# Kernel tuning notes

Measured on AMD Instinct MI355X. Metric: run time of the kernel, lower is better.

## Reference

```python
import jax, jax.numpy as jnp
import numpy as np

N_NODES = 50000
N_EDGES = 800000
IN_FEATS = 64
HIDDEN = 64
NUM_CLASSES = 32


def _graph_conv(x, src, dst, W, b, n_nodes):
    # DGL GraphConv, norm='both', allow_zero_in_degree=True:
    # out = D_in^{-1/2} * (A^T @ (D_out^{-1/2} * x)) @ W + b, degrees clamped to >=1
    e = src.shape[0]
    ones = jnp.ones((e,), dtype=x.dtype)
    out_deg = jax.ops.segment_sum(ones, src, num_segments=n_nodes)
    in_deg = jax.ops.segment_sum(ones, dst, num_segments=n_nodes)
    norm_src = jax.lax.rsqrt(jnp.maximum(out_deg, 1.0))[:, None]
    norm_dst = jax.lax.rsqrt(jnp.maximum(in_deg, 1.0))[:, None]
    h = x * norm_src                                   # [N, d]
    agg = jax.ops.segment_sum(h[src], dst, num_segments=n_nodes)  # gather+scatter over edges
    return (agg * norm_dst) @ W + b


def setup_inputs() -> dict:
    key = jax.random.key(0)
    k1, k2, k3, k4, k5 = jax.random.split(key, 5)
    features = jax.random.normal(k1, (N_NODES, IN_FEATS), dtype=jnp.float32)
    src = jax.random.randint(k2, (N_EDGES,), 0, N_NODES, dtype=jnp.int32)
    dst = jax.random.randint(k3, (N_EDGES,), 0, N_NODES, dtype=jnp.int32)
    W1 = jax.random.normal(k4, (IN_FEATS, HIDDEN), dtype=jnp.float32) * (1.0 / np.sqrt(IN_FEATS))
    b1 = jnp.zeros((HIDDEN,), dtype=jnp.float32)
    W2 = jax.random.normal(k5, (HIDDEN, NUM_CLASSES), dtype=jnp.float32) * (1.0 / np.sqrt(HIDDEN))
    b2 = jnp.zeros((NUM_CLASSES,), dtype=jnp.float32)
    return {"features": features, "src": src, "dst": dst,
            "W1": W1, "b1": b1, "W2": W2, "b2": b2}


def reference(features, src, dst, W1, b1, W2, b2) -> jnp.ndarray:
    n = features.shape[0]
    h = jax.nn.relu(_graph_conv(features, src, dst, W1, b1, n))
    out = _graph_conv(h, src, dst, W2, b2, n)
    # single canonical etype -> mean over one-element stack is identity
    return out
```

## Files before the change

kernel.cpp:

```cpp
#include <hip/hip_runtime.h>
#include <hip/hip_bf16.h>

#define N_NODES 50000
#define N_EDGES 800000
#define F 64
#define C 32
#define CAP 48

#define NPB   200
#define EPB   4000
#define NBUCK 196

#define G1_BLOCKS   2048
#define GOUT_BLOCKS 2048

static __device__ __forceinline__ float bflo(int u) {
    return __uint_as_float(((unsigned)u) << 16);
}
static __device__ __forceinline__ float bfhi(int u) {
    return __uint_as_float(((unsigned)u) & 0xffff0000u);
}
static __device__ __forceinline__ unsigned short f2bf(float f) {
    __hip_bfloat16 h = __float2bfloat16(f);
    return *reinterpret_cast<unsigned short*>(&h);
}

__global__ void part_count_kernel(const int* __restrict__ src, const int* __restrict__ dst,
                                  int* __restrict__ bcnt_d, int* __restrict__ bcnt_s) {
    __shared__ int hd[NBUCK], hs[NBUCK];
    int t = threadIdx.x;
    for (int i = t; i < NBUCK; i += 256) { hd[i] = 0; hs[i] = 0; }
    __syncthreads();
    int b0 = blockIdx.x * EPB;
    for (int i = b0 + t; i < b0 + EPB; i += 256) {
        atomicAdd(&hd[dst[i] >> 8], 1);
        atomicAdd(&hs[src[i] >> 8], 1);
    }
    __syncthreads();
    for (int i = t; i < NBUCK; i += 256) {
        bcnt_d[i * NPB + blockIdx.x] = hd[i];
        bcnt_s[i * NPB + blockIdx.x] = hs[i];
    }
}

__global__ void part_scan_kernel(const int* __restrict__ bcnt_d, const int* __restrict__ bcnt_s,
                                 int* __restrict__ eoff_d, int* __restrict__ eoff_s,
                                 int* __restrict__ base_d, int* __restrict__ base_s) {
    __shared__ int tot_d[NBUCK], tot_s[NBUCK], bd[NBUCK + 1], bs[NBUCK + 1];
    int t = threadIdx.x;
    if (t < NBUCK) {
        int run = 0;
        for (int q = 0; q < NPB / 4; q++) {
            int4 v = *reinterpret_cast<const int4*>(bcnt_d + t * NPB + 4 * q);
            int4 o;
            o.x = run; run += v.x;
            o.y = run; run += v.y;
            o.z = run; run += v.z;
            o.w = run; run += v.w;
            *reinterpret_cast<int4*>(eoff_d + t * NPB + 4 * q) = o;
        }
        tot_d[t] = run;
        run = 0;
        for (int q = 0; q < NPB / 4; q++) {
            int4 v = *reinterpret_cast<const int4*>(bcnt_s + t * NPB + 4 * q);
            int4 o;
            o.x = run; run += v.x;
            o.y = run; run += v.y;
            o.z = run; run += v.z;
            o.w = run; run += v.w;
            *reinterpret_cast<int4*>(eoff_s + t * NPB + 4 * q) = o;
        }
        tot_s[t] = run;
    }
    __syncthreads();
    if (t == 0) {
        int r = 0;
        for (int b = 0; b < NBUCK; b++) { bd[b] = r; r += tot_d[b]; }
        bd[NBUCK] = r;
        r = 0;
        for (int b = 0; b < NBUCK; b++) { bs[b] = r; r += tot_s[b]; }
        bs[NBUCK] = r;
    }
    __syncthreads();
    if (t < NBUCK + 1) { base_d[t] = bd[t]; base_s[t] = bs[t]; }
}

__global__ void part_scatter_kernel(const int* __restrict__ src, const int* __restrict__ dst,
                                    const int* __restrict__ eoff_d, const int* __restrict__ eoff_s,
                                    const int* __restrict__ base_d, const int* __restrict__ base_s,
                                    int* __restrict__ edge_d, unsigned char* __restrict__ edge_s) {
    __shared__ int cd[NBUCK], cs[NBUCK];
    int t = threadIdx.x;
    for (int i = t; i < NBUCK; i += 256) {
        cd[i] = base_d[i] + eoff_d[i * NPB + blockIdx.x];
        cs[i] = base_s[i] + eoff_s[i * NPB + blockIdx.x];
    }
    __syncthreads();
    int b0 = blockIdx.x * EPB;
    for (int i = b0 + t; i < b0 + EPB; i += 256) {
        int d = dst[i], s = src[i];
        int p = atomicAdd(&cd[d >> 8], 1);
        edge_d[p] = ((d & 255) << 16) | s;
        int q = atomicAdd(&cs[s >> 8], 1);
        edge_s[q] = (unsigned char)(s & 255);
    }
}

__global__ void bucket_build_kernel(const int* __restrict__ edge_d,
                                    const unsigned char* __restrict__ edge_s,
                                    const int* __restrict__ base_d, const int* __restrict__ base_s,
                                    int* __restrict__ csr, int* __restrict__ cnt,
                                    float* __restrict__ norm_dst, float* __restrict__ norm_src) {
    __shared__ int cur[256];
    __shared__ int hs[256];
    int t = threadIdx.x;
    int bucket = blockIdx.x;
    cur[t] = 0;
    hs[t] = 0;
    __syncthreads();
    int lo = base_d[bucket], hi = base_d[bucket + 1];
    for (int i = lo + t; i < hi; i += 256) {
        int pd = edge_d[i];
        int dlow = pd >> 16;
        int s = pd & 0xFFFF;
        int pos = atomicAdd(&cur[dlow], 1);
        if (pos < CAP) csr[(size_t)(bucket * 256 + dlow) * CAP + pos] = s;
    }
    int slo = base_s[bucket], shi = base_s[bucket + 1];
    for (int i = slo + t; i < shi; i += 256) {
        atomicAdd(&hs[edge_s[i]], 1);
    }
    __syncthreads();
    int node = bucket * 256 + t;
    if (node < N_NODES) {
        int c = cur[t] < CAP ? cur[t] : CAP;
        cnt[node] = c;
        norm_dst[node] = rsqrtf(fmaxf((float)c, 1.0f));
        norm_src[node] = rsqrtf(fmaxf((float)hs[t], 1.0f));
    }
}

__global__ void gemm_y_kernel(const float* __restrict__ x,
                              const float* __restrict__ ns,
                              const float* __restrict__ W,
                              __hip_bfloat16* __restrict__ y) {
    __shared__ float sW[F * F];
    __shared__ float srow[16][F];
    int t = threadIdx.x;
    for (int i = t; i < F * F; i += 256) sW[i] = W[i];
    int j = t & 63;
    int w = t >> 6;
    int base = blockIdx.x * 16;
    for (int r = w; r < 16; r += 4) srow[r][j] = x[(size_t)(base + r) * F + j];
    __syncthreads();
    float a0 = 0, a1 = 0, a2 = 0, a3 = 0;
#pragma unroll
    for (int k = 0; k < F; k++) {
        float wv = sW[k * F + j];
        a0 += srow[w * 4 + 0][k] * wv;
        a1 += srow[w * 4 + 1][k] * wv;
        a2 += srow[w * 4 + 2][k] * wv;
        a3 += srow[w * 4 + 3][k] * wv;
    }
    int n0 = base + w * 4;
    y[(size_t)(n0 + 0) * F + j] = __float2bfloat16(a0 * ns[n0 + 0]);
    y[(size_t)(n0 + 1) * F + j] = __float2bfloat16(a1 * ns[n0 + 1]);
    y[(size_t)(n0 + 2) * F + j] = __float2bfloat16(a2 * ns[n0 + 2]);
    y[(size_t)(n0 + 3) * F + j] = __float2bfloat16(a3 * ns[n0 + 3]);
}

__global__ void gather64_gemv_kernel(const __hip_bfloat16* __restrict__ y,
                                     const int* __restrict__ csr,
                                     const int* __restrict__ cnt,
                                     const float* __restrict__ norm_dst,
                                     const float* __restrict__ norm_src,
                                     const float* __restrict__ b1,
                                     const float* __restrict__ W2,
                                     __hip_bfloat16* __restrict__ gt) {
    __shared__ float sW[F * C];
    int t = threadIdx.x;
    for (int i = t; i < F * C; i += 256) sW[i] = W2[i];
    __syncthreads();
    int w    = t >> 6;
    int lane = t & 63;
    int g  = lane >> 3;
    int fo = (lane & 7) * 8;
    int j    = lane & 31;
    int half = lane >> 5;
    const float4 b1a = *reinterpret_cast<const float4*>(b1 + fo);
    const float4 b1b = *reinterpret_cast<const float4*>(b1 + fo + 4);
    const unsigned short* ytab = reinterpret_cast<const unsigned short*>(y);
    const int STRIDE = G1_BLOCKS * 4;

    int node = blockIdx.x * 4 + w;
    int pn = cnt[node];
    float pnd = norm_dst[node], pns = norm_src[node];
    const int* prow = csr + (size_t)node * CAP;
    int pr0 = prow[g],      pr1 = prow[8 + g],  pr2 = prow[16 + g];
    int pr3 = prow[24 + g], pr4 = prow[32 + g], pr5 = prow[40 + g];

    while (node < N_NODES) {
        int n = pn;
        float nd = pnd, ns = pns;
        int r0 = pr0, r1 = pr1, r2 = pr2, r3 = pr3, r4 = pr4, r5 = pr5;
        int nxt = node + STRIDE;
        int pf = (nxt < N_NODES) ? nxt : node;

        int ss0 = (g      < n) ? r0 : 0;  float m0 = (g      < n) ? 1.f : 0.f;
        int ss1 = (8  + g < n) ? r1 : 0;  float m1 = (8  + g < n) ? 1.f : 0.f;
        int ss2 = (16 + g < n) ? r2 : 0;  float m2 = (16 + g < n) ? 1.f : 0.f;
        int ss3 = (24 + g < n) ? r3 : 0;  float m3 = (24 + g < n) ? 1.f : 0.f;
        int ss4 = (32 + g < n) ? r4 : 0;  float m4 = (32 + g < n) ? 1.f : 0.f;
        int ss5 = (40 + g < n) ? r5 : 0;  float m5 = (40 + g < n) ? 1.f : 0.f;

        const int4 v0 = *reinterpret_cast<const int4*>(ytab + (size_t)ss0 * F + fo);
        const int4 v1 = *reinterpret_cast<const int4*>(ytab + (size_t)ss1 * F + fo);
        const int4 v2 = *reinterpret_cast<const int4*>(ytab + (size_t)ss2 * F + fo);
        const int4 v3 = *reinterpret_cast<const int4*>(ytab + (size_t)ss3 * F + fo);

        pn  = cnt[pf];
        pnd = norm_dst[pf];
        pns = norm_src[pf];
        const int* nrow = csr + (size_t)pf * CAP;
        pr0 = nrow[g];      pr1 = nrow[8 + g];  pr2 = nrow[16 + g];
        pr3 = nrow[24 + g]; pr4 = nrow[32 + g]; pr5 = nrow[40 + g];

        float a0, a1, a2, a3, a4, a5, a6, a7;
        a0 = m0 * bflo(v0.x); a1 = m0 * bfhi(v0.x);
        a2 = m0 * bflo(v0.y); a3 = m0 * bfhi(v0.y);
        a4 = m0 * bflo(v0.z); a5 = m0 * bfhi(v0.z);
        a6 = m0 * bflo(v0.w); a7 = m0 * bfhi(v0.w);

        const int4 v4 = *reinterpret_cast<const int4*>(ytab + (size_t)ss4 * F + fo);
        const int4 v5 = *reinterpret_cast<const int4*>(ytab + (size_t)ss5 * F + fo);

#define G1_ACC(vv, mm)                                                        \
        a0 = fmaf(mm, bflo(vv.x), a0); a1 = fmaf(mm, bfhi(vv.x), a1);         \
        a2 = fmaf(mm, bflo(vv.y), a2); a3 = fmaf(mm, bfhi(vv.y), a3);         \
        a4 = fmaf(mm, bflo(vv.z), a4); a5 = fmaf(mm, bfhi(vv.z), a5);         \
        a6 = fmaf(mm, bflo(vv.w), a6); a7 = fmaf(mm, bfhi(vv.w), a7);
        G1_ACC(v1, m1)
        G1_ACC(v2, m2)
        G1_ACC(v3, m3)
        G1_ACC(v4, m4)
        G1_ACC(v5, m5)
#undef G1_ACC

#define G1_RED(mk)                                                           \
        a0 += __shfl_xor(a0, mk); a1 += __shfl_xor(a1, mk);                  \
        a2 += __shfl_xor(a2, mk); a3 += __shfl_xor(a3, mk);                  \
        a4 += __shfl_xor(a4, mk); a5 += __shfl_xor(a5, mk);                  \
        a6 += __shfl_xor(a6, mk); a7 += __shfl_xor(a7, mk);
        G1_RED(8)
        G1_RED(16)
        G1_RED(32)
#undef G1_RED

        float hh[8];
        hh[0] = fmaxf(fmaf(a0, nd, b1a.x), 0.f) * ns;
        hh[1] = fmaxf(fmaf(a1, nd, b1a.y), 0.f) * ns;
        hh[2] = fmaxf(fmaf(a2, nd, b1a.z), 0.f) * ns;
        hh[3] = fmaxf(fmaf(a3, nd, b1a.w), 0.f) * ns;
        hh[4] = fmaxf(fmaf(a4, nd, b1b.x), 0.f) * ns;
        hh[5] = fmaxf(fmaf(a5, nd, b1b.y), 0.f) * ns;
        hh[6] = fmaxf(fmaf(a6, nd, b1b.z), 0.f) * ns;
        hh[7] = fmaxf(fmaf(a7, nd, b1b.w), 0.f) * ns;

        float o = 0.f;
#pragma unroll
        for (int k = 0; k < 32; k++) {
            float hv = __shfl(hh[k & 7], (half << 2) + (k >> 3));
            o = fmaf(hv, sW[(half * 32 + k) * C + j], o);
        }
        o += __shfl_down(o, 32);
        if (half == 0)
            __builtin_nontemporal_store(f2bf(o),
                reinterpret_cast<unsigned short*>(gt) + (size_t)node * C + j);
        node = nxt;
    }
}

__global__ void gather_out_kernel(const __hip_bfloat16* __restrict__ gt,
                                  const int* __restrict__ csr,
                                  const int* __restrict__ cnt,
                                  const float* __restrict__ norm_dst,
                                  const float* __restrict__ b2,
                                  float* __restrict__ out) {
    int t = threadIdx.x;
    int w = t >> 6;
    int lane = t & 63;
    int g  = lane >> 3;
    int fo = (lane & 7) * 4;
    const unsigned short* tab = reinterpret_cast<const unsigned short*>(gt);
    const float4 bb = *reinterpret_cast<const float4*>(b2 + fo);
    const int STRIDE = GOUT_BLOCKS * 4;

    int node = blockIdx.x * 4 + w;
    int pn = cnt[node];
    float pnd = norm_dst[node];
    const int* prow = csr + (size_t)node * CAP;
    int pr0 = prow[g],      pr1 = prow[8 + g],  pr2 = prow[16 + g];
    int pr3 = prow[24 + g], pr4 = prow[32 + g], pr5 = prow[40 + g];

    while (node < N_NODES) {
        int n = pn;
        float nd = pnd;
        int r0 = pr0, r1 = pr1, r2 = pr2, r3 = pr3, r4 = pr4, r5 = pr5;
        int nxt = node + STRIDE;
        int pf = (nxt < N_NODES) ? nxt : node;

        int ss0 = (g      < n) ? r0 : 0;  float m0 = (g      < n) ? 1.f : 0.f;
        int ss1 = (8  + g < n) ? r1 : 0;  float m1 = (8  + g < n) ? 1.f : 0.f;
        int ss2 = (16 + g < n) ? r2 : 0;  float m2 = (16 + g < n) ? 1.f : 0.f;
        int ss3 = (24 + g < n) ? r3 : 0;  float m3 = (24 + g < n) ? 1.f : 0.f;
        int ss4 = (32 + g < n) ? r4 : 0;  float m4 = (32 + g < n) ? 1.f : 0.f;
        int ss5 = (40 + g < n) ? r5 : 0;  float m5 = (40 + g < n) ? 1.f : 0.f;

        const int2 v0 = *reinterpret_cast<const int2*>(tab + (size_t)ss0 * C + fo);
        const int2 v1 = *reinterpret_cast<const int2*>(tab + (size_t)ss1 * C + fo);
        const int2 v2 = *reinterpret_cast<const int2*>(tab + (size_t)ss2 * C + fo);
        const int2 v3 = *reinterpret_cast<const int2*>(tab + (size_t)ss3 * C + fo);

        pn  = cnt[pf];
        pnd = norm_dst[pf];
        const int* nrow = csr + (size_t)pf * CAP;
        pr0 = nrow[g];      pr1 = nrow[8 + g];  pr2 = nrow[16 + g];
        pr3 = nrow[24 + g]; pr4 = nrow[32 + g]; pr5 = nrow[40 + g];

        float a0, a1, a2, a3;
        a0 = m0 * bflo(v0.x); a1 = m0 * bfhi(v0.x);
        a2 = m0 * bflo(v0.y); a3 = m0 * bfhi(v0.y);

        const int2 v4 = *reinterpret_cast<const int2*>(tab + (size_t)ss4 * C + fo);
        const int2 v5 = *reinterpret_cast<const int2*>(tab + (size_t)ss5 * C + fo);

#define G2_ACC(vv, mm)                                                        \
        a0 = fmaf(mm, bflo(vv.x), a0); a1 = fmaf(mm, bfhi(vv.x), a1);         \
        a2 = fmaf(mm, bflo(vv.y), a2); a3 = fmaf(mm, bfhi(vv.y), a3);
        G2_ACC(v1, m1)
        G2_ACC(v2, m2)
        G2_ACC(v3, m3)
        G2_ACC(v4, m4)
        G2_ACC(v5, m5)
#undef G2_ACC

        a0 += __shfl_xor(a0, 8);  a1 += __shfl_xor(a1, 8);
        a2 += __shfl_xor(a2, 8);  a3 += __shfl_xor(a3, 8);
        a0 += __shfl_xor(a0, 16); a1 += __shfl_xor(a1, 16);
        a2 += __shfl_xor(a2, 16); a3 += __shfl_xor(a3, 16);
        a0 += __shfl_xor(a0, 32); a1 += __shfl_xor(a1, 32);
        a2 += __shfl_xor(a2, 32); a3 += __shfl_xor(a3, 32);

        if (lane < 8) {
            float o0 = fmaf(a0, nd, bb.x);
            float o1 = fmaf(a1, nd, bb.y);
            float o2 = fmaf(a2, nd, bb.z);
            float o3 = fmaf(a3, nd, bb.w);
            unsigned long long p0 = ((unsigned long long)__float_as_uint(o0)) |
                                    ((unsigned long long)__float_as_uint(o1) << 32);
            unsigned long long p1 = ((unsigned long long)__float_as_uint(o2)) |
                                    ((unsigned long long)__float_as_uint(o3) << 32);
            unsigned long long* po = reinterpret_cast<unsigned long long*>(
                out + (size_t)node * C + fo);
            __builtin_nontemporal_store(p0, po);
            __builtin_nontemporal_store(p1, po + 1);
        }
        node = nxt;
    }
}

extern "C" void kernel_launch(void* const* d_in, const int* in_sizes, int n_in,
                              void* d_out, int out_size, void* d_ws, size_t ws_size,
                              hipStream_t stream) {
    const float* features = (const float*)d_in[0];
    const int*   src      = (const int*)d_in[1];
    const int*   dst      = (const int*)d_in[2];
    const float* W1       = (const float*)d_in[3];
    const float* b1       = (const float*)d_in[4];
    const float* W2       = (const float*)d_in[5];
    const float* b2       = (const float*)d_in[6];
    float* out = (float*)d_out;

    char* p = (char*)d_ws;
    float* norm_src = (float*)p;  p += (size_t)N_NODES * 4;
    float* norm_dst = (float*)p;  p += (size_t)N_NODES * 4;
    int*   cnt      = (int*)p;    p += (size_t)N_NODES * 4;
    int*   csr      = (int*)p;    p += (size_t)N_NODES * CAP * 4;
    __hip_bfloat16* y  = (__hip_bfloat16*)p;  p += (size_t)N_NODES * F * 2;
    __hip_bfloat16* gt = (__hip_bfloat16*)p;

    int* edge_d = (int*)y;
    unsigned char* edge_s = (unsigned char*)(edge_d + N_EDGES);
    int* q = (int*)gt;
    int* bcnt_d = q;                 q += NPB * NBUCK;
    int* bcnt_s = q;                 q += NPB * NBUCK;
    int* eoff_d = q;                 q += NPB * NBUCK;
    int* eoff_s = q;                 q += NPB * NBUCK;
    int* base_d = q;                 q += NBUCK + 1;
    int* base_s = q;

    part_count_kernel<<<NPB, 256, 0, stream>>>(src, dst, bcnt_d, bcnt_s);
    part_scan_kernel<<<1, 256, 0, stream>>>(bcnt_d, bcnt_s, eoff_d, eoff_s, base_d, base_s);
    part_scatter_kernel<<<NPB, 256, 0, stream>>>(src, dst, eoff_d, eoff_s, base_d, base_s,
                                                 edge_d, edge_s);
    bucket_build_kernel<<<NBUCK, 256, 0, stream>>>(edge_d, edge_s, base_d, base_s,
                                                   csr, cnt, norm_dst, norm_src);

    gemm_y_kernel<<<N_NODES / 16, 256, 0, stream>>>(features, norm_src, W1, y);
    gather64_gemv_kernel<<<G1_BLOCKS, 256, 0, stream>>>(y, csr, cnt, norm_dst,
                                                        norm_src, b1, W2, gt);

    gather_out_kernel<<<GOUT_BLOCKS, 256, 0, stream>>>(gt, csr, cnt, norm_dst,
                                                       b2, out);
}
```

Baseline: 210.0 us.

## Vectorize partition passes, parallel-scan buckets, pack node metadata, skip rare high-degree gathers

The edge partition count and scatter kernels now read src/dst as int4, and the single-thread bucket prefix scan becomes a shared-memory Hillis-Steele scan. Per-node count, norm_dst and norm_src are packed into one float4 meta array, so each node needs one 16-byte load instead of three scattered ones. Both gather kernels prefetch only the first 32 neighbour indices and load slots 32-47 in a branch taken only when degree exceeds 32. This cuts index traffic and register pressure on the common path, at the cost of a divergent extra load on high-degree nodes.

Result: faster. 196.4 us (-6.5%).

```diff
diff --git a/kernel.cpp b/kernel.cpp
--- a/kernel.cpp
+++ b/kernel.cpp
@@ -32,9 +32,15 @@
     for (int i = t; i < NBUCK; i += 256) { hd[i] = 0; hs[i] = 0; }
     __syncthreads();
     int b0 = blockIdx.x * EPB;
-    for (int i = b0 + t; i < b0 + EPB; i += 256) {
-        atomicAdd(&hd[dst[i] >> 8], 1);
-        atomicAdd(&hs[src[i] >> 8], 1);
+    const int4* s4 = reinterpret_cast<const int4*>(src + b0);
+    const int4* d4 = reinterpret_cast<const int4*>(dst + b0);
+    for (int i = t; i < EPB / 4; i += 256) {
+        int4 dv = d4[i];
+        int4 sv = s4[i];
+        atomicAdd(&hd[dv.x >> 8], 1); atomicAdd(&hd[dv.y >> 8], 1);
+        atomicAdd(&hd[dv.z >> 8], 1); atomicAdd(&hd[dv.w >> 8], 1);
+        atomicAdd(&hs[sv.x >> 8], 1); atomicAdd(&hs[sv.y >> 8], 1);
+        atomicAdd(&hs[sv.z >> 8], 1); atomicAdd(&hs[sv.w >> 8], 1);
     }
     __syncthreads();
     for (int i = t; i < NBUCK; i += 256) {
@@ -46,8 +52,8 @@
 __global__ void part_scan_kernel(const int* __restrict__ bcnt_d, const int* __restrict__ bcnt_s,
                                  int* __restrict__ eoff_d, int* __restrict__ eoff_s,
                                  int* __restrict__ base_d, int* __restrict__ base_s) {
-    __shared__ int tot_d[NBUCK], tot_s[NBUCK], bd[NBUCK + 1], bs[NBUCK + 1];
-    int t = threadIdx.x;
+    int t = threadIdx.x;
+    int vd = 0, vs = 0;
     if (t < NBUCK) {
         int run = 0;
         for (int q = 0; q < NPB / 4; q++) {
@@ -59,7 +65,7 @@
             o.w = run; run += v.w;
             *reinterpret_cast<int4*>(eoff_d + t * NPB + 4 * q) = o;
         }
-        tot_d[t] = run;
+        vd = run;
         run = 0;
         for (int q = 0; q < NPB / 4; q++) {
             int4 v = *reinterpret_cast<const int4*>(bcnt_s + t * NPB + 4 * q);
@@ -70,19 +76,20 @@
             o.w = run; run += v.w;
             *reinterpret_cast<int4*>(eoff_s + t * NPB + 4 * q) = o;
         }
-        tot_s[t] = run;
-    }
-    __syncthreads();
-    if (t == 0) {
-        int r = 0;
-        for (int b = 0; b < NBUCK; b++) { bd[b] = r; r += tot_d[b]; }
-        bd[NBUCK] = r;
-        r = 0;
-        for (int b = 0; b < NBUCK; b++) { bs[b] = r; r += tot_s[b]; }
-        bs[NBUCK] = r;
-    }
-    __syncthreads();
-    if (t < NBUCK + 1) { base_d[t] = bd[t]; base_s[t] = bs[t]; }
+        vs = run;
+    }
+    __shared__ int sd[256], ss[256];
+    sd[t] = vd; ss[t] = vs;
+    __syncthreads();
+    for (int off = 1; off < 256; off <<= 1) {
+        int ad = (t >= off) ? sd[t - off] : 0;
+        int as = (t >= off) ? ss[t - off] : 0;
+        __syncthreads();
+        sd[t] += ad; ss[t] += as;
+        __syncthreads();
+    }
+    if (t < NBUCK) { base_d[t] = sd[t] - vd; base_s[t] = ss[t] - vs; }
+    if (t == NBUCK - 1) { base_d[NBUCK] = sd[t]; base_s[NBUCK] = ss[t]; }
 }
 
 __global__ void part_scatter_kernel(const int* __restrict__ src, const int* __restrict__ dst,
@@ -97,20 +104,27 @@
     }
     __syncthreads();
     int b0 = blockIdx.x * EPB;
-    for (int i = b0 + t; i < b0 + EPB; i += 256) {
-        int d = dst[i], s = src[i];
-        int p = atomicAdd(&cd[d >> 8], 1);
-        edge_d[p] = ((d & 255) << 16) | s;
-        int q = atomicAdd(&cs[s >> 8], 1);
-        edge_s[q] = (unsigned char)(s & 255);
+    const int4* s4 = reinterpret_cast<const int4*>(src + b0);
+    const int4* d4 = reinterpret_cast<const int4*>(dst + b0);
+    for (int i = t; i < EPB / 4; i += 256) {
+        int4 dv = d4[i];
+        int4 sv = s4[i];
+        int p;
+        p = atomicAdd(&cd[dv.x >> 8], 1); edge_d[p] = ((dv.x & 255) << 16) | sv.x;
+        p = atomicAdd(&cd[dv.y >> 8], 1); edge_d[p] = ((dv.y & 255) << 16) | sv.y;
+        p = atomicAdd(&cd[dv.z >> 8], 1); edge_d[p] = ((dv.z & 255) << 16) | sv.z;
+        p = atomicAdd(&cd[dv.w >> 8], 1); edge_d[p] = ((dv.w & 255) << 16) | sv.w;
+        p = atomicAdd(&cs[sv.x >> 8], 1); edge_s[p] = (unsigned char)(sv.x & 255);
+        p = atomicAdd(&cs[sv.y >> 8], 1); edge_s[p] = (unsigned char)(sv.y & 255);
+        p = atomicAdd(&cs[sv.z >> 8], 1); edge_s[p] = (unsigned char)(sv.z & 255);
+        p = atomicAdd(&cs[sv.w >> 8], 1); edge_s[p] = (unsigned char)(sv.w & 255);
     }
 }
 
 __global__ void bucket_build_kernel(const int* __restrict__ edge_d,
                                     const unsigned char* __restrict__ edge_s,
                                     const int* __restrict__ base_d, const int* __restrict__ base_s,
-                                    int* __restrict__ csr, int* __restrict__ cnt,
-                                    float* __restrict__ norm_dst, float* __restrict__ norm_src) {
+                                    int* __restrict__ csr, float4* __restrict__ meta) {
     __shared__ int cur[256];
     __shared__ int hs[256];
     int t = threadIdx.x;
@@ -134,14 +148,17 @@
     int node = bucket * 256 + t;
     if (node < N_NODES) {
         int c = cur[t] < CAP ? cur[t] : CAP;
-        cnt[node] = c;
-        norm_dst[node] = rsqrtf(fmaxf((float)c, 1.0f));
-        norm_src[node] = rsqrtf(fmaxf((float)hs[t], 1.0f));
+        float4 m;
+        m.x = rsqrtf(fmaxf((float)c, 1.0f));
+        m.y = rsqrtf(fmaxf((float)hs[t], 1.0f));
+        m.z = __int_as_float(c);
+        m.w = 0.f;
+        meta[node] = m;
     }
 }
 
 __global__ void gemm_y_kernel(const float* __restrict__ x,
-                              const float* __restrict__ ns,
+                              const float4* __restrict__ meta,
                               const float* __restrict__ W,
                               __hip_bfloat16* __restrict__ y) {
     __shared__ float sW[F * F];
@@ -163,17 +180,15 @@
         a3 += srow[w * 4 + 3][k] * wv;
     }
     int n0 = base + w * 4;
-    y[(size_t)(n0 + 0) * F + j] = __float2bfloat16(a0 * ns[n0 + 0]);
-    y[(size_t)(n0 + 1) * F + j] = __float2bfloat16(a1 * ns[n0 + 1]);
-    y[(size_t)(n0 + 2) * F + j] = __float2bfloat16(a2 * ns[n0 + 2]);
-    y[(size_t)(n0 + 3) * F + j] = __float2bfloat16(a3 * ns[n0 + 3]);
+    y[(size_t)(n0 + 0) * F + j] = __float2bfloat16(a0 * meta[n0 + 0].y);
+    y[(size_t)(n0 + 1) * F + j] = __float2bfloat16(a1 * meta[n0 + 1].y);
+    y[(size_t)(n0 + 2) * F + j] = __float2bfloat16(a2 * meta[n0 + 2].y);
+    y[(size_t)(n0 + 3) * F + j] = __float2bfloat16(a3 * meta[n0 + 3].y);
 }
 
 __global__ void gather64_gemv_kernel(const __hip_bfloat16* __restrict__ y,
                                      const int* __restrict__ csr,
-                                     const int* __restrict__ cnt,
-                                     const float* __restrict__ norm_dst,
-                                     const float* __restrict__ norm_src,
+                                     const float4* __restrict__ meta,
                                      const float* __restrict__ b1,
                                      const float* __restrict__ W2,
                                      __hip_bfloat16* __restrict__ gt) {
@@ -193,16 +208,14 @@
     const int STRIDE = G1_BLOCKS * 4;
 
     int node = blockIdx.x * 4 + w;
-    int pn = cnt[node];
-    float pnd = norm_dst[node], pns = norm_src[node];
+    float4 pm = meta[node];
     const int* prow = csr + (size_t)node * CAP;
-    int pr0 = prow[g],      pr1 = prow[8 + g],  pr2 = prow[16 + g];
-    int pr3 = prow[24 + g], pr4 = prow[32 + g], pr5 = prow[40 + g];
+    int pr0 = prow[g], pr1 = prow[8 + g], pr2 = prow[16 + g], pr3 = prow[24 + g];
 
     while (node < N_NODES) {
-        int n = pn;
-        float nd = pnd, ns = pns;
-        int r0 = pr0, r1 = pr1, r2 = pr2, r3 = pr3, r4 = pr4, r5 = pr5;
+        float nd = pm.x, ns = pm.y;
+        int n = __float_as_int(pm.z);
+        int r0 = pr0, r1 = pr1, r2 = pr2, r3 = pr3;
         int nxt = node + STRIDE;
         int pf = (nxt < N_NODES) ? nxt : node;
 
@@ -210,29 +223,21 @@
         int ss1 = (8  + g < n) ? r1 : 0;  float m1 = (8  + g < n) ? 1.f : 0.f;
         int ss2 = (16 + g < n) ? r2 : 0;  float m2 = (16 + g < n) ? 1.f : 0.f;
         int ss3 = (24 + g < n) ? r3 : 0;  float m3 = (24 + g < n) ? 1.f : 0.f;
-        int ss4 = (32 + g < n) ? r4 : 0;  float m4 = (32 + g < n) ? 1.f : 0.f;
-        int ss5 = (40 + g < n) ? r5 : 0;  float m5 = (40 + g < n) ? 1.f : 0.f;
 
         const int4 v0 = *reinterpret_cast<const int4*>(ytab + (size_t)ss0 * F + fo);
         const int4 v1 = *reinterpret_cast<const int4*>(ytab + (size_t)ss1 * F + fo);
         const int4 v2 = *reinterpret_cast<const int4*>(ytab + (size_t)ss2 * F + fo);
         const int4 v3 = *reinterpret_cast<const int4*>(ytab + (size_t)ss3 * F + fo);
 
-        pn  = cnt[pf];
-        pnd = norm_dst[pf];
-        pns = norm_src[pf];
+        pm = meta[pf];
         const int* nrow = csr + (size_t)pf * CAP;
-        pr0 = nrow[g];      pr1 = nrow[8 + g];  pr2 = nrow[16 + g];
-        pr3 = nrow[24 + g]; pr4 = nrow[32 + g]; pr5 = nrow[40 + g];
+        pr0 = nrow[g]; pr1 = nrow[8 + g]; pr2 = nrow[16 + g]; pr3 = nrow[24 + g];
 
         float a0, a1, a2, a3, a4, a5, a6, a7;
         a0 = m0 * bflo(v0.x); a1 = m0 * bfhi(v0.x);
         a2 = m0 * bflo(v0.y); a3 = m0 * bfhi(v0.y);
         a4 = m0 * bflo(v0.z); a5 = m0 * bfhi(v0.z);
         a6 = m0 * bflo(v0.w); a7 = m0 * bfhi(v0.w);
-
-        const int4 v4 = *reinterpret_cast<const int4*>(ytab + (size_t)ss4 * F + fo);
-        const int4 v5 = *reinterpret_cast<const int4*>(ytab + (size_t)ss5 * F + fo);
 
 #define G1_ACC(vv, mm)                                                        \
         a0 = fmaf(mm, bflo(vv.x), a0); a1 = fmaf(mm, bfhi(vv.x), a1);         \
@@ -242,8 +247,17 @@
         G1_ACC(v1, m1)
         G1_ACC(v2, m2)
         G1_ACC(v3, m3)
-        G1_ACC(v4, m4)
-        G1_ACC(v5, m5)
+
+        if (__builtin_expect(n > 32, 0)) {
+            const int* row = csr + (size_t)node * CAP;
+            int r4 = row[32 + g], r5 = row[40 + g];
+            int ss4 = (32 + g < n) ? r4 : 0;  float m4 = (32 + g < n) ? 1.f : 0.f;
+            int ss5 = (40 + g < n) ? r5 : 0;  float m5 = (40 + g < n) ? 1.f : 0.f;
+            const int4 v4 = *reinterpret_cast<const int4*>(ytab + (size_t)ss4 * F + fo);
+            const int4 v5 = *reinterpret_cast<const int4*>(ytab + (size_t)ss5 * F + fo);
+            G1_ACC(v4, m4)
+            G1_ACC(v5, m5)
+        }
 #undef G1_ACC
 
 #define G1_RED(mk)                                                           \
@@ -282,8 +296,7 @@
 
 __global__ void gather_out_kernel(const __hip_bfloat16* __restrict__ gt,
                                   const int* __restrict__ csr,
-                                  const int* __restrict__ cnt,
-                                  const float* __restrict__ norm_dst,
+                                  const float4* __restrict__ meta,
                                   const float* __restrict__ b2,
                                   float* __restrict__ out) {
     int t = threadIdx.x;
@@ -296,16 +309,14 @@
     const int STRIDE = GOUT_BLOCKS * 4;
 
     int node = blockIdx.x * 4 + w;
-    int pn = cnt[node];
-    float pnd = norm_dst[node];
+    float4 pm = meta[node];
     const int* prow = csr + (size_t)node * CAP;
-    int pr0 = prow[g],      pr1 = prow[8 + g],  pr2 = prow[16 + g];
-    int pr3 = prow[24 + g], pr4 = prow[32 + g], pr5 = prow[40 + g];
+    int pr0 = prow[g], pr1 = prow[8 + g], pr2 = prow[16 + g], pr3 = prow[24 + g];
 
     while (node < N_NODES) {
-        int n = pn;
-        float nd = pnd;
-        int r0 = pr0, r1 = pr1, r2 = pr2, r3 = pr3, r4 = pr4, r5 = pr5;
+        float nd = pm.x;
+        int n = __float_as_int(pm.z);
+        int r0 = pr0, r1 = pr1, r2 = pr2, r3 = pr3;
         int nxt = node + STRIDE;
         int pf = (nxt < N_NODES) ? nxt : node;
 
@@ -313,26 +324,19 @@
         int ss1 = (8  + g < n) ? r1 : 0;  float m1 = (8  + g < n) ? 1.f : 0.f;
         int ss2 = (16 + g < n) ? r2 : 0;  float m2 = (16 + g < n) ? 1.f : 0.f;
         int ss3 = (24 + g < n) ? r3 : 0;  float m3 = (24 + g < n) ? 1.f : 0.f;
-        int ss4 = (32 + g < n) ? r4 : 0;  float m4 = (32 + g < n) ? 1.f : 0.f;
-        int ss5 = (40 + g < n) ? r5 : 0;  float m5 = (40 + g < n) ? 1.f : 0.f;
 
         const int2 v0 = *reinterpret_cast<const int2*>(tab + (size_t)ss0 * C + fo);
         const int2 v1 = *reinterpret_cast<const int2*>(tab + (size_t)ss1 * C + fo);
         const int2 v2 = *reinterpret_cast<const int2*>(tab + (size_t)ss2 * C + fo);
         const int2 v3 = *reinterpret_cast<const int2*>(tab + (size_t)ss3 * C + fo);
 
-        pn  = cnt[pf];
-        pnd = norm_dst[pf];
+        pm = meta[pf];
         const int* nrow = csr + (size_t)pf * CAP;
-        pr0 = nrow[g];      pr1 = nrow[8 + g];  pr2 = nrow[16 + g];
-        pr3 = nrow[24 + g]; pr4 = nrow[32 + g]; pr5 = nrow[40 + g];
+        pr0 = nrow[g]; pr1 = nrow[8 + g]; pr2 = nrow[16 + g]; pr3 = nrow[24 + g];
 
         float a0, a1, a2, a3;
         a0 = m0 * bflo(v0.x); a1 = m0 * bfhi(v0.x);
         a2 = m0 * bflo(v0.y); a3 = m0 * bfhi(v0.y);
-
-        const int2 v4 = *reinterpret_cast<const int2*>(tab + (size_t)ss4 * C + fo);
-        const int2 v5 = *reinterpret_cast<const int2*>(tab + (size_t)ss5 * C + fo);
 
 #define G2_ACC(vv, mm)                                                        \
         a0 = fmaf(mm, bflo(vv.x), a0); a1 = fmaf(mm, bfhi(vv.x), a1);         \
@@ -340,8 +344,17 @@
         G2_ACC(v1, m1)
         G2_ACC(v2, m2)
         G2_ACC(v3, m3)
-        G2_ACC(v4, m4)
-        G2_ACC(v5, m5)
+
+        if (__builtin_expect(n > 32, 0)) {
+            const int* row = csr + (size_t)node * CAP;
+            int r4 = row[32 + g], r5 = row[40 + g];
+            int ss4 = (32 + g < n) ? r4 : 0;  float m4 = (32 + g < n) ? 1.f : 0.f;
+            int ss5 = (40 + g < n) ? r5 : 0;  float m5 = (40 + g < n) ? 1.f : 0.f;
+            const int2 v4 = *reinterpret_cast<const int2*>(tab + (size_t)ss4 * C + fo);
+            const int2 v5 = *reinterpret_cast<const int2*>(tab + (size_t)ss5 * C + fo);
+            G2_ACC(v4, m4)
+            G2_ACC(v5, m5)
+        }
 #undef G2_ACC
 
         a0 += __shfl_xor(a0, 8);  a1 += __shfl_xor(a1, 8);
@@ -382,10 +395,8 @@
     float* out = (float*)d_out;
 
     char* p = (char*)d_ws;
-    float* norm_src = (float*)p;  p += (size_t)N_NODES * 4;
-    float* norm_dst = (float*)p;  p += (size_t)N_NODES * 4;
-    int*   cnt      = (int*)p;    p += (size_t)N_NODES * 4;
-    int*   csr      = (int*)p;    p += (size_t)N_NODES * CAP * 4;
+    float4* meta = (float4*)p;    p += (size_t)N_NODES * 16;
+    int*    csr  = (int*)p;       p += (size_t)N_NODES * CAP * 4;
     __hip_bfloat16* y  = (__hip_bfloat16*)p;  p += (size_t)N_NODES * F * 2;
     __hip_bfloat16* gt = (__hip_bfloat16*)p;
 
@@ -404,12 +415,10 @@
     part_scatter_kernel<<<NPB, 256, 0, stream>>>(src, dst, eoff_d, eoff_s, base_d, base_s,
                                                  edge_d, edge_s);
     bucket_build_kernel<<<NBUCK, 256, 0, stream>>>(edge_d, edge_s, base_d, base_s,
-                                                   csr, cnt, norm_dst, norm_src);
-
-    gemm_y_kernel<<<N_NODES / 16, 256, 0, stream>>>(features, norm_src, W1, y);
-    gather64_gemv_kernel<<<G1_BLOCKS, 256, 0, stream>>>(y, csr, cnt, norm_dst,
-                                                        norm_src, b1, W2, gt);
-
-    gather_out_kernel<<<GOUT_BLOCKS, 256, 0, stream>>>(gt, csr, cnt, norm_dst,
-                                                       b2, out);
-}
+                                                   csr, meta);
+
+    gemm_y_kernel<<<N_NODES / 16, 256, 0, stream>>>(features, meta, W1, y);
+    gather64_gemv_kernel<<<G1_BLOCKS, 256, 0, stream>>>(y, csr, meta, b1, W2, gt);
+
+    gather_out_kernel<<<GOUT_BLOCKS, 256, 0, stream>>>(gt, csr, meta, b2, out);
+}
```
